# Kernel optimization log

Hardware: AMD Instinct MI355X
Metric: run time of the kernel (lower is better)

Reference implementation:

```python
import jax, jax.numpy as jnp
import numpy as np

B, T, D, H = 8, 2048, 512, 128

def setup_inputs() -> dict:
    key = jax.random.key(0)
    ks = jax.random.split(key, 8)
    s = lambda fan_in: 1.0 / np.sqrt(fan_in)
    return {
        "x": jax.random.normal(ks[0], (B, T, D), jnp.float32),
        "prediction": jax.random.normal(ks[1], (B, T, D), jnp.float32),
        "Wq": jax.random.uniform(ks[2], (D, H), jnp.float32, -s(D), s(D)),
        "bq": jnp.zeros((H,), jnp.float32),
        "Wk": jax.random.uniform(ks[3], (D, H), jnp.float32, -s(D), s(D)),
        "bk": jnp.zeros((H,), jnp.float32),
        "Wv": jax.random.uniform(ks[4], (D, D), jnp.float32, -s(D), s(D)),
        "bv": jnp.zeros((D,), jnp.float32),
        "Wf": jax.random.uniform(ks[5], (2 * D, D), jnp.float32, -s(2 * D), s(2 * D)),
        "bf": jnp.zeros((D,), jnp.float32),
    }

def reference(x, prediction, Wq, bq, Wk, bk, Wv, bv, Wf, bf):
    # q,k: [B,T,H]; v: [B,T,D]
    q = jnp.einsum('btd,dh->bth', prediction, Wq) + bq
    k = jnp.einsum('btd,dh->bth', x, Wk) + bk
    v = jnp.einsum('btd,de->bte', x, Wv) + bv
    # unscaled attention scores [B,T,T]
    scores = jnp.einsum('bth,bsh->bts', q, k)
    attn = jax.nn.softmax(scores, axis=-1)
    attended = jnp.einsum('bts,bsd->btd', attn, v)
    fusion_input = jnp.concatenate([prediction, attended], axis=-1)  # [B,T,2D]
    return jax.nn.sigmoid(jnp.einsum('btf,fd->btd', fusion_input, Wf) + bf)
```

## Files before the change

### kernel.cpp

```cpp
#include <hip/hip_runtime.h>
#include <hip/hip_bf16.h>


#define APF_B 8
#define APF_T 2048
#define APF_D 512
#define APF_H 128
#define APF_M (APF_B * APF_T)

typedef unsigned short u16;
typedef __attribute__((ext_vector_type(8))) short short8;
typedef __attribute__((ext_vector_type(4))) float f32x4;
typedef __attribute__((ext_vector_type(16))) float f32x16;

static __device__ __forceinline__ u16 f2bf(float x) {
    union { float f; unsigned int u; } cv;
    cv.f = x;
    unsigned int u = cv.u + 0x7FFFu + ((cv.u >> 16) & 1u);
    return (u16)(u >> 16);
}
static __device__ __forceinline__ u16 f2bf_hw(float x) {
    union { __hip_bfloat16 h; u16 u; } cv;
    cv.h = __float2bfloat16(x);
    return cv.u;
}

static __device__ __forceinline__ void load16_lds(const u16* g, u16* l) {
    __builtin_amdgcn_global_load_lds(
        (const __attribute__((address_space(1))) unsigned int*)g,
        (__attribute__((address_space(3))) unsigned int*)l,
        16, 0, 0);
}

static __device__ __forceinline__ f32x16 zero16() {
    f32x16 v;
#pragma unroll
    for (int i = 0; i < 16; ++i) v[i] = 0.f;
    return v;
}

__global__ __launch_bounds__(256) void prep_w(
    const float* __restrict__ Wq, u16* __restrict__ WqT,
    const float* __restrict__ Wk, u16* __restrict__ WkT,
    const float* __restrict__ Wv, u16* __restrict__ WvT,
    const float* __restrict__ Wf, u16* __restrict__ WfT)
{
    __shared__ float tile[64][65];
    int b = blockIdx.x;
    const float* src; u16* dst; int K, N;
    if (b < 16)      { src = Wq; dst = WqT; K = 512;  N = 128; }
    else if (b < 32) { b -= 16; src = Wk; dst = WkT; K = 512;  N = 128; }
    else if (b < 96) { b -= 32; src = Wv; dst = WvT; K = 512;  N = 512; }
    else             { b -= 96; src = Wf; dst = WfT; K = 1024; N = 512; }
    const int ntN = N >> 6;
    const int k0 = (b / ntN) * 64, n0 = (b % ntN) * 64;

    const int tid = threadIdx.x;
#pragma unroll
    for (int rep = 0; rep < 4; ++rep) {
        const int r = (tid >> 4) + rep * 16;
        const int c = (tid & 15) * 4;
        const float4 v = *(const float4*)&src[(long)(k0 + r) * N + n0 + c];
        tile[r][c] = v.x; tile[r][c + 1] = v.y;
        tile[r][c + 2] = v.z; tile[r][c + 3] = v.w;
    }
    __syncthreads();
#pragma unroll
    for (int rep = 0; rep < 2; ++rep) {
        const int rn = (tid >> 3) + rep * 32;
        const int ck = (tid & 7) * 8;
        short8 o;
#pragma unroll
        for (int j = 0; j < 8; ++j)
            o[j] = (short)f2bf_hw(tile[ck + j][rn]);
        *(short8*)&dst[(long)(n0 + rn) * K + k0 + ck] = o;
    }
}

template <int ADT, int BDT, int EPI, int BIASM, int VBLK>
static __device__ __forceinline__ void gemm_body(
    u16 (&smA)[2][4096], u16 (&smB)[2][4096],
    const void* Ap, long lda,
    const void* Bp, long ldb,
    const float* bias, void* Cp, long ldc, int K,
    long row0, long col0, const float* Cadd)
{
    const int tid  = threadIdx.x;
    const int lane = tid & 63;
    const int wid  = tid >> 6;
    const int wr   = wid >> 1;
    const int wc   = wid & 1;

    f32x4 acc[4][4];
#pragma unroll
    for (int i = 0; i < 4; ++i)
#pragma unroll
        for (int j = 0; j < 4; ++j)
            acc[i][j] = (f32x4){0.f, 0.f, 0.f, 0.f};

    const int lrow = (lane >> 4) * 4;
    const int lcol = lane & 15;
    const int q8   = (lane >> 4) * 8;

    float4 ra[2][2], rb[2][2];

    auto loadA = [&](int kb) {
        if (ADT == 1) {
            const float* Af = (const float*)Ap;
#pragma unroll
            for (int rep = 0; rep < 2; ++rep) {
                const int c = tid + rep * 256;
                const int rr = c >> 2, kc = (c & 3) * 8;
                const float* ga = Af + (row0 + rr) * lda + kb + kc;
                ra[rep][0] = *(const float4*)ga;
                ra[rep][1] = *(const float4*)(ga + 4);
            }
        }
    };
    auto loadB = [&](int kb) {
        if (BDT == 1) {
            const float* Bf = (const float*)Bp;
#pragma unroll
            for (int rep = 0; rep < 2; ++rep) {
                const int c = tid + rep * 256;
                const int rr = c >> 2, kc = (c & 3) * 8;
                const float* gb = Bf + (col0 + rr) * ldb + kb + kc;
                rb[rep][0] = *(const float4*)gb;
                rb[rep][1] = *(const float4*)(gb + 4);
            }
        }
    };
    auto dmaA = [&](int buf, int kb) {
        if (ADT == 0) {
            const u16* Ab = (const u16*)Ap;
#pragma unroll
            for (int rep = 0; rep < 2; ++rep) {
                const int c = tid + rep * 256;
                const int rr = c >> 2, kc = (c & 3) * 8;
                const int wbase = (wid * 64 + rep * 256) * 8;
                load16_lds(Ab + (row0 + rr) * lda + kb + kc, &smA[buf][wbase]);
            }
        }
    };
    auto dmaB = [&](int buf, int kb) {
        if (BDT == 0) {
            const u16* Bb = (const u16*)Bp;
#pragma unroll
            for (int rep = 0; rep < 2; ++rep) {
                const int c = tid + rep * 256;
                const int rr = c >> 2, kc = (c & 3) * 8;
                const int wbase = (wid * 64 + rep * 256) * 8;
                load16_lds(Bb + (col0 + rr) * ldb + kb + kc, &smB[buf][wbase]);
            }
        }
    };
    auto cvt8 = [&](const float4& a, const float4& b) {
        short8 v;
        v[0] = (short)f2bf_hw(a.x); v[1] = (short)f2bf_hw(a.y);
        v[2] = (short)f2bf_hw(a.z); v[3] = (short)f2bf_hw(a.w);
        v[4] = (short)f2bf_hw(b.x); v[5] = (short)f2bf_hw(b.y);
        v[6] = (short)f2bf_hw(b.z); v[7] = (short)f2bf_hw(b.w);
        return v;
    };
    auto writeA = [&](int buf) {
        if (ADT == 1) {
#pragma unroll
            for (int rep = 0; rep < 2; ++rep) {
                const int c = tid + rep * 256;
                *(short8*)&smA[buf][c * 8] = cvt8(ra[rep][0], ra[rep][1]);
            }
        }
    };
    auto writeB = [&](int buf) {
        if (BDT == 1) {
#pragma unroll
            for (int rep = 0; rep < 2; ++rep) {
                const int c = tid + rep * 256;
                *(short8*)&smB[buf][c * 8] = cvt8(rb[rep][0], rb[rep][1]);
            }
        }
    };

    const int NT = K / 32;
    loadA(0); loadB(0);
    writeA(0); writeB(0);
    dmaA(0, 0); dmaB(0, 0);

    int cur = 0;
    for (int t = 0; t < NT; ++t) {
        const int kb2 = (t + 1) * 32;
        if (t + 1 < NT) { loadA(kb2); loadB(kb2); }
        __syncthreads();
        if (t + 1 < NT) { dmaA(cur ^ 1, kb2); dmaB(cur ^ 1, kb2); }

        short8 av[4], bv4[4];
#pragma unroll
        for (int ti = 0; ti < 4; ++ti)
            av[ti] = *(const short8*)&smA[cur][(wr * 64 + ti * 16 + lcol) * 32 + q8];
#pragma unroll
        for (int tj = 0; tj < 4; ++tj)
            bv4[tj] = *(const short8*)&smB[cur][(wc * 64 + tj * 16 + lcol) * 32 + q8];

#pragma unroll
        for (int ti = 0; ti < 4; ++ti)
#pragma unroll
            for (int tj = 0; tj < 4; ++tj)
                acc[ti][tj] = __builtin_amdgcn_mfma_f32_16x16x32_bf16(
                    av[ti], bv4[tj], acc[ti][tj], 0, 0, 0);

        if (t + 1 < NT) { writeA(cur ^ 1); writeB(cur ^ 1); }
        cur ^= 1;
    }

#pragma unroll
    for (int ti = 0; ti < 4; ++ti) {
        const long m0t = row0 + wr * 64 + ti * 16 + lrow;
#pragma unroll
        for (int tj = 0; tj < 4; ++tj) {
            const long n = col0 + wc * 64 + tj * 16 + lcol;
            const float bn = (BIASM == 0 && bias != nullptr) ? bias[n] : 0.f;
            if (EPI == 0) {
                u16* C = (u16*)Cp;
#pragma unroll
                for (int r = 0; r < 4; ++r) {
                    const long m = m0t + r;
                    const float bm = (BIASM == 1) ? bias[m] : bn;
                    long idx;
                    if (VBLK) {
                        idx = ((((m >> 5) * 256) + (n >> 3)) << 8) +
                              ((m & 31) << 3) + (n & 7);
                    } else {
                        idx = m * ldc + n;
                    }
                    C[idx] = f2bf(acc[ti][tj][r] + bm);
                }
            } else if (EPI == 2) {
                float* C = (float*)Cp;
#pragma unroll
                for (int r = 0; r < 4; ++r) {
                    const float val = acc[ti][tj][r] + bn;
                    C[(m0t + r) * ldc + n] = 1.0f / (1.0f + expf(-val));
                }
            } else if (EPI == 3) {
                float* C = (float*)Cp;
#pragma unroll
                for (int r = 0; r < 4; ++r)
                    C[(m0t + r) * ldc + n] = acc[ti][tj][r] + bn;
            } else {
                float* C = (float*)Cp;
#pragma unroll
                for (int r = 0; r < 4; ++r) {
                    const float val = acc[ti][tj][r] + Cadd[(m0t + r) * ldc + n];
                    C[(m0t + r) * ldc + n] = 1.0f / (1.0f + expf(-val));
                }
            }
        }
    }
}

__global__ __launch_bounds__(256, 3) void mid_gemms(
    const float* __restrict__ x, const float* __restrict__ pred,
    const u16* __restrict__ WqT, const u16* __restrict__ WkT,
    const u16* __restrict__ WvT, const u16* __restrict__ WfT,
    const float* __restrict__ bq, const float* __restrict__ bk,
    const float* __restrict__ bv, const float* __restrict__ bfu,
    u16* __restrict__ qb, u16* __restrict__ kbuf, u16* __restrict__ vTb,
    float* __restrict__ Cpre)
{
    __shared__ u16 smA[2][4096];
    __shared__ u16 smB[2][4096];

    const int bid = blockIdx.x;
    if (bid < 256) {
        const int zz = bid >> 7, by = bid & 127;
        gemm_body<1, 0, 0, 0, 0>(smA, smB,
            zz ? (const void*)x : (const void*)pred, APF_D,
            zz ? WkT : WqT, APF_D,
            zz ? bk : bq, zz ? (void*)kbuf : (void*)qb, APF_H, APF_D,
            (long)by * 128, 0, nullptr);
    } else if (bid < 768) {
        const int t = bid - 256;
        const int zz = t >> 6, rem = t & 63;
        const int bx = rem & 15, by = rem >> 4;
        gemm_body<0, 1, 0, 1, 1>(smA, smB,
            WvT, APF_D,
            (const void*)(x + (long)zz * APF_T * APF_D), APF_D,
            bv, (void*)(vTb + (long)zz * 1048576L), APF_T, APF_D,
            (long)by * 128, (long)bx * 128, nullptr);
    } else {
        const int t = bid - 768;
        const int bx = t & 3, by = t >> 2;
        gemm_body<1, 0, 3, 0, 0>(smA, smB,
            (const void*)pred, APF_D,
            WfT, 1024,
            bfu, (void*)Cpre, APF_D, APF_D,
            (long)by * 128, (long)bx * 128, nullptr);
    }
}

__global__ __launch_bounds__(256, 2) void fusion_gemm(
    const u16* __restrict__ attb, const u16* __restrict__ WfT,
    const float* __restrict__ Cpre, float* __restrict__ out)
{
    __shared__ u16 smA[2][4096];
    __shared__ u16 smB[2][4096];
    gemm_body<0, 0, 4, 0, 0>(smA, smB,
        (const void*)attb, APF_D,
        WfT + 512, 1024,
        nullptr, (void*)out, APF_D, APF_D,
        (long)blockIdx.y * 128, (long)blockIdx.x * 128, Cpre);
}

__global__ __launch_bounds__(256, 3) void attn_fused(
    const u16* __restrict__ qg, const u16* __restrict__ kg,
    const u16* __restrict__ vTg, u16* __restrict__ attg)
{
    __shared__ u16 sQ[64 * 128];
    __shared__ u16 sK[64 * 128];
    __shared__ u16 sP[64 * 64];
    __shared__ float sRS[192];

    const int tid  = threadIdx.x;
    const int lane = tid & 63;
    const int w    = tid >> 6;
    const int l31  = lane & 31;
    const int hi   = lane >> 5;
    const int qb   = w >> 1;
    const int sb   = w & 1;

    const int  bid = blockIdx.x;
    const long z   = bid & 7;
    const int  r   = bid >> 3;
    const long q0  = (long)(r & 31) * 64;
    const long d0  = (long)(r >> 5) * 256;

    const u16* kbase0 = kg + z * (long)APF_T * APF_H;

    {
        const u16* qsrc = qg + (z * APF_T + q0) * APF_H;
#pragma unroll
        for (int rep = 0; rep < 4; ++rep) {
            const int c    = tid + rep * 256;
            const int row  = c >> 4;
            const int col8 = (c & 15) * 8;
            load16_lds(qsrc + row * APF_H + (col8 ^ ((row & 15) << 3)), &sQ[c * 8]);
        }
#pragma unroll
        for (int rep = 0; rep < 4; ++rep) {
            const int c    = tid + rep * 256;
            const int row  = c >> 4;
            const int col8 = (c & 15) * 8;
            load16_lds(kbase0 + row * APF_H + (col8 ^ ((row & 15) << 3)), &sK[c * 8]);
        }
    }
    __syncthreads();

    f32x16 oacc[2][2];
#pragma unroll
    for (int i = 0; i < 2; ++i)
#pragma unroll
        for (int j = 0; j < 2; ++j) oacc[i][j] = zero16();
    f32x16 rsacc = zero16();

    const long dblk0 = (d0 >> 5) + w * 2;
    const u16* vzb = vTg + z * 1048576L + dblk0 * 65536L + (long)l31 * 8;

    const int qrow = qb * 32 + l31;
    const int krow = sb * 32 + l31;
    const int pcol = sb * 32 + l31;

    for (int kt = 0; kt < APF_T / 64; ++kt) {
        f32x16 sacc = zero16();
#pragma unroll
        for (int ks = 0; ks < 8; ++ks) {
            const int colk = ks * 16 + hi * 8;
            const short8 av = *(const short8*)&sQ[qrow * 128 + (colk ^ ((qrow & 15) << 3))];
            const short8 bv = *(const short8*)&sK[krow * 128 + (colk ^ ((krow & 15) << 3))];
            sacc = __builtin_amdgcn_mfma_f32_32x32x16_bf16(av, bv, sacc, 0, 0, 0);
        }
        __syncthreads();

        if (kt + 1 < APF_T / 64) {
            const u16* ksrc = kbase0 + (long)(kt + 1) * 64 * APF_H;
#pragma unroll
            for (int rep = 0; rep < 4; ++rep) {
                const int c    = tid + rep * 256;
                const int row  = c >> 4;
                const int col8 = (c & 15) * 8;
                load16_lds(ksrc + row * APF_H + (col8 ^ ((row & 15) << 3)), &sK[c * 8]);
            }
        }

        const long sbase = (long)kt * 8 + hi;
        short8 vf1[2][2];
#pragma unroll
        for (int dt = 0; dt < 2; ++dt)
#pragma unroll
            for (int ks = 0; ks < 2; ++ks)
                vf1[dt][ks] = *(const short8*)(vzb + dt * 65536L + (sbase + ks * 2) * 256);

#pragma unroll
        for (int rg = 0; rg < 16; ++rg) {
            const float e = __expf(sacc[rg]);
            rsacc[rg] += e;
            const int prow = qb * 32 + (rg & 3) + 8 * (rg >> 2) + 4 * hi;
            sP[prow * 64 + (pcol ^ ((prow & 7) << 3))] = f2bf(e);
        }
        __syncthreads();

#pragma unroll
        for (int ks = 0; ks < 2; ++ks) {
            const int colk = ks * 16 + hi * 8;
            short8 pa[2];
#pragma unroll
            for (int qt = 0; qt < 2; ++qt) {
                const int prow = qt * 32 + l31;
                pa[qt] = *(const short8*)&sP[prow * 64 + (colk ^ ((prow & 7) << 3))];
            }
#pragma unroll
            for (int dt = 0; dt < 2; ++dt)
#pragma unroll
                for (int qt = 0; qt < 2; ++qt)
                    oacc[qt][dt] = __builtin_amdgcn_mfma_f32_32x32x16_bf16(
                        pa[qt], vf1[dt][ks], oacc[qt][dt], 0, 0, 0);
        }

        short8 vf2[2][2];
#pragma unroll
        for (int dt = 0; dt < 2; ++dt)
#pragma unroll
            for (int ks = 0; ks < 2; ++ks)
                vf2[dt][ks] = *(const short8*)(vzb + dt * 65536L + (sbase + (ks + 2) * 2) * 256);

#pragma unroll
        for (int ks = 0; ks < 2; ++ks) {
            const int colk = (ks + 2) * 16 + hi * 8;
            short8 pa[2];
#pragma unroll
            for (int qt = 0; qt < 2; ++qt) {
                const int prow = qt * 32 + l31;
                pa[qt] = *(const short8*)&sP[prow * 64 + (colk ^ ((prow & 7) << 3))];
            }
#pragma unroll
            for (int dt = 0; dt < 2; ++dt)
#pragma unroll
                for (int qt = 0; qt < 2; ++qt)
                    oacc[qt][dt] = __builtin_amdgcn_mfma_f32_32x32x16_bf16(
                        pa[qt], vf2[dt][ks], oacc[qt][dt], 0, 0, 0);
        }
    }

#pragma unroll
    for (int rg = 0; rg < 16; ++rg) {
        float s = rsacc[rg];
        s += __shfl_xor(s, 1);
        s += __shfl_xor(s, 2);
        s += __shfl_xor(s, 4);
        s += __shfl_xor(s, 8);
        s += __shfl_xor(s, 16);
        rsacc[rg] = s;
    }
    if (l31 == 0) {
#pragma unroll
        for (int rg = 0; rg < 16; ++rg) {
            const int row = (rg & 3) + 8 * (rg >> 2) + 4 * hi;
            sRS[w * 32 + row] = rsacc[rg];
        }
    }
    __syncthreads();
    if (tid < 64) {
        const int qb2 = tid >> 5, r2 = tid & 31;
        sRS[128 + tid] = 1.0f / (sRS[(qb2 * 2 + 0) * 32 + r2] +
                                 sRS[(qb2 * 2 + 1) * 32 + r2]);
    }
    __syncthreads();

    const long rowg0 = z * APF_T + q0;
    const long colg0 = d0 + (long)w * 64;
#pragma unroll
    for (int qt = 0; qt < 2; ++qt)
#pragma unroll
        for (int rg = 0; rg < 16; ++rg) {
            const int row = qt * 32 + (rg & 3) + 8 * (rg >> 2) + 4 * hi;
            const float inv = sRS[128 + row];
#pragma unroll
            for (int dt = 0; dt < 2; ++dt)
                attg[(rowg0 + row) * APF_D + colg0 + dt * 32 + l31] =
                    f2bf(oacc[qt][dt][rg] * inv);
        }
}

extern "C" void kernel_launch(void* const* d_in, const int* in_sizes, int n_in,
                              void* d_out, int out_size, void* d_ws, size_t ws_size,
                              hipStream_t stream)
{
    (void)in_sizes; (void)n_in; (void)out_size; (void)ws_size;

    const float* x    = (const float*)d_in[0];
    const float* pred = (const float*)d_in[1];
    const float* Wq   = (const float*)d_in[2];
    const float* bq   = (const float*)d_in[3];
    const float* Wk   = (const float*)d_in[4];
    const float* bk   = (const float*)d_in[5];
    const float* Wv   = (const float*)d_in[6];
    const float* bv   = (const float*)d_in[7];
    const float* Wf   = (const float*)d_in[8];
    const float* bfu  = (const float*)d_in[9];

    float* Cpre = (float*)d_ws;
    u16* wsp  = (u16*)(Cpre + (long)APF_M * APF_D);
    u16* qb   = wsp;
    u16* kbuf = qb   + (long)APF_M * APF_H;
    u16* vTb  = kbuf + (long)APF_M * APF_H;
    u16* attb = vTb  + (long)APF_M * APF_D;
    u16* WqT  = attb + (long)APF_M * APF_D;
    u16* WkT  = WqT  + (long)APF_H * APF_D;
    u16* WvT  = WkT  + (long)APF_H * APF_D;
    u16* WfT  = WvT  + (long)APF_D * APF_D;

    const dim3 thr(256);

    prep_w<<<dim3(224), thr, 0, stream>>>(Wq, WqT, Wk, WkT, Wv, WvT, Wf, WfT);

    mid_gemms<<<dim3(1280), thr, 0, stream>>>(
        x, pred, WqT, WkT, WvT, WfT, bq, bk, bv, bfu, qb, kbuf, vTb, Cpre);

    attn_fused<<<dim3(512), thr, 0, stream>>>(qb, kbuf, vTb, attb);

    fusion_gemm<<<dim3(4, 128), thr, 0, stream>>>(attb, WfT, Cpre,
                                                  (float*)d_out);
}
```

Measured before the change: 254.3 us.

## Double-buffer K and P tiles in attention, hold Q in registers, swizzle GEMM LDS

The attention kernel now keeps its Q fragments in registers instead of shared memory and double-buffers the K and P shared-memory tiles. This removes one of the two block barriers per key tile, and all V fragments are loaded in one batch. The GEMM body applies an XOR swizzle to its LDS tile layout for both DMA and converted stores, to cut bank conflicts on fragment reads. In exchange the attention kernel uses more registers and shared memory, and its launch bound drops from 3 to 2 blocks per CU.

```diff
diff --git a/kernel.cpp b/kernel.cpp
--- a/kernel.cpp
+++ b/kernel.cpp
@@ -7,6 +7,8 @@
 #define APF_D 512
 #define APF_H 128
 #define APF_M (APF_B * APF_T)
+
+#define GSWZ(row) ((((row) >> 1) & 3) << 3)
 
 typedef unsigned short u16;
 typedef __attribute__((ext_vector_type(8))) short short8;
@@ -138,7 +140,8 @@
                 const int c = tid + rep * 256;
                 const int rr = c >> 2, kc = (c & 3) * 8;
                 const int wbase = (wid * 64 + rep * 256) * 8;
-                load16_lds(Ab + (row0 + rr) * lda + kb + kc, &smA[buf][wbase]);
+                load16_lds(Ab + (row0 + rr) * lda + kb + (kc ^ GSWZ(rr)),
+                           &smA[buf][wbase]);
             }
         }
     };
@@ -150,7 +153,8 @@
                 const int c = tid + rep * 256;
                 const int rr = c >> 2, kc = (c & 3) * 8;
                 const int wbase = (wid * 64 + rep * 256) * 8;
-                load16_lds(Bb + (col0 + rr) * ldb + kb + kc, &smB[buf][wbase]);
+                load16_lds(Bb + (col0 + rr) * ldb + kb + (kc ^ GSWZ(rr)),
+                           &smB[buf][wbase]);
             }
         }
     };
@@ -167,7 +171,8 @@
 #pragma unroll
             for (int rep = 0; rep < 2; ++rep) {
                 const int c = tid + rep * 256;
-                *(short8*)&smA[buf][c * 8] = cvt8(ra[rep][0], ra[rep][1]);
+                *(short8*)&smA[buf][(c * 8) ^ GSWZ(c >> 2)] =
+                    cvt8(ra[rep][0], ra[rep][1]);
             }
         }
     };
@@ -176,7 +181,8 @@
 #pragma unroll
             for (int rep = 0; rep < 2; ++rep) {
                 const int c = tid + rep * 256;
-                *(short8*)&smB[buf][c * 8] = cvt8(rb[rep][0], rb[rep][1]);
+                *(short8*)&smB[buf][(c * 8) ^ GSWZ(c >> 2)] =
+                    cvt8(rb[rep][0], rb[rep][1]);
             }
         }
     };
@@ -195,11 +201,15 @@
 
         short8 av[4], bv4[4];
 #pragma unroll
-        for (int ti = 0; ti < 4; ++ti)
-            av[ti] = *(const short8*)&smA[cur][(wr * 64 + ti * 16 + lcol) * 32 + q8];
-#pragma unroll
-        for (int tj = 0; tj < 4; ++tj)
-            bv4[tj] = *(const short8*)&smB[cur][(wc * 64 + tj * 16 + lcol) * 32 + q8];
+        for (int ti = 0; ti < 4; ++ti) {
+            const int arow = wr * 64 + ti * 16 + lcol;
+            av[ti] = *(const short8*)&smA[cur][arow * 32 + (q8 ^ GSWZ(arow))];
+        }
+#pragma unroll
+        for (int tj = 0; tj < 4; ++tj) {
+            const int brow = wc * 64 + tj * 16 + lcol;
+            bv4[tj] = *(const short8*)&smB[cur][brow * 32 + (q8 ^ GSWZ(brow))];
+        }
 
 #pragma unroll
         for (int ti = 0; ti < 4; ++ti)
@@ -311,13 +321,12 @@
         (long)blockIdx.y * 128, (long)blockIdx.x * 128, Cpre);
 }
 
-__global__ __launch_bounds__(256, 3) void attn_fused(
+__global__ __launch_bounds__(256, 2) void attn_fused(
     const u16* __restrict__ qg, const u16* __restrict__ kg,
     const u16* __restrict__ vTg, u16* __restrict__ attg)
 {
-    __shared__ u16 sQ[64 * 128];
-    __shared__ u16 sK[64 * 128];
-    __shared__ u16 sP[64 * 64];
+    __shared__ u16 sK[2][64 * 128];
+    __shared__ u16 sP[2][64 * 64];
     __shared__ float sRS[192];
 
     const int tid  = threadIdx.x;
@@ -336,22 +345,21 @@
 
     const u16* kbase0 = kg + z * (long)APF_T * APF_H;
 
+#pragma unroll
+    for (int rep = 0; rep < 4; ++rep) {
+        const int c    = tid + rep * 256;
+        const int row  = c >> 4;
+        const int col8 = (c & 15) * 8;
+        load16_lds(kbase0 + row * APF_H + (col8 ^ ((row & 15) << 3)),
+                   &sK[0][c * 8]);
+    }
+
+    short8 qf[8];
     {
-        const u16* qsrc = qg + (z * APF_T + q0) * APF_H;
-#pragma unroll
-        for (int rep = 0; rep < 4; ++rep) {
-            const int c    = tid + rep * 256;
-            const int row  = c >> 4;
-            const int col8 = (c & 15) * 8;
-            load16_lds(qsrc + row * APF_H + (col8 ^ ((row & 15) << 3)), &sQ[c * 8]);
-        }
-#pragma unroll
-        for (int rep = 0; rep < 4; ++rep) {
-            const int c    = tid + rep * 256;
-            const int row  = c >> 4;
-            const int col8 = (c & 15) * 8;
-            load16_lds(kbase0 + row * APF_H + (col8 ^ ((row & 15) << 3)), &sK[c * 8]);
-        }
+        const u16* qsrc = qg + (z * APF_T + q0 + qb * 32 + l31) * APF_H;
+#pragma unroll
+        for (int ks = 0; ks < 8; ++ks)
+            qf[ks] = *(const short8*)(qsrc + ks * 16 + hi * 8);
     }
     __syncthreads();
 
@@ -365,20 +373,19 @@
     const long dblk0 = (d0 >> 5) + w * 2;
     const u16* vzb = vTg + z * 1048576L + dblk0 * 65536L + (long)l31 * 8;
 
-    const int qrow = qb * 32 + l31;
     const int krow = sb * 32 + l31;
     const int pcol = sb * 32 + l31;
 
+    int cur = 0;
     for (int kt = 0; kt < APF_T / 64; ++kt) {
         f32x16 sacc = zero16();
 #pragma unroll
         for (int ks = 0; ks < 8; ++ks) {
             const int colk = ks * 16 + hi * 8;
-            const short8 av = *(const short8*)&sQ[qrow * 128 + (colk ^ ((qrow & 15) << 3))];
-            const short8 bv = *(const short8*)&sK[krow * 128 + (colk ^ ((krow & 15) << 3))];
-            sacc = __builtin_amdgcn_mfma_f32_32x32x16_bf16(av, bv, sacc, 0, 0, 0);
-        }
-        __syncthreads();
+            const short8 bv =
+                *(const short8*)&sK[cur][krow * 128 + (colk ^ ((krow & 15) << 3))];
+            sacc = __builtin_amdgcn_mfma_f32_32x32x16_bf16(qf[ks], bv, sacc, 0, 0, 0);
+        }
 
         if (kt + 1 < APF_T / 64) {
             const u16* ksrc = kbase0 + (long)(kt + 1) * 64 * APF_H;
@@ -387,67 +394,45 @@
                 const int c    = tid + rep * 256;
                 const int row  = c >> 4;
                 const int col8 = (c & 15) * 8;
-                load16_lds(ksrc + row * APF_H + (col8 ^ ((row & 15) << 3)), &sK[c * 8]);
+                load16_lds(ksrc + row * APF_H + (col8 ^ ((row & 15) << 3)),
+                           &sK[cur ^ 1][c * 8]);
             }
         }
 
         const long sbase = (long)kt * 8 + hi;
-        short8 vf1[2][2];
+        short8 vf[2][4];
 #pragma unroll
         for (int dt = 0; dt < 2; ++dt)
 #pragma unroll
-            for (int ks = 0; ks < 2; ++ks)
-                vf1[dt][ks] = *(const short8*)(vzb + dt * 65536L + (sbase + ks * 2) * 256);
+            for (int ks = 0; ks < 4; ++ks)
+                vf[dt][ks] = *(const short8*)(vzb + dt * 65536L + (sbase + ks * 2) * 256);
 
 #pragma unroll
         for (int rg = 0; rg < 16; ++rg) {
             const float e = __expf(sacc[rg]);
             rsacc[rg] += e;
             const int prow = qb * 32 + (rg & 3) + 8 * (rg >> 2) + 4 * hi;
-            sP[prow * 64 + (pcol ^ ((prow & 7) << 3))] = f2bf(e);
+            sP[cur][prow * 64 + (pcol ^ ((prow & 7) << 3))] = f2bf(e);
         }
         __syncthreads();
 
 #pragma unroll
-        for (int ks = 0; ks < 2; ++ks) {
+        for (int ks = 0; ks < 4; ++ks) {
             const int colk = ks * 16 + hi * 8;
             short8 pa[2];
 #pragma unroll
             for (int qt = 0; qt < 2; ++qt) {
                 const int prow = qt * 32 + l31;
-                pa[qt] = *(const short8*)&sP[prow * 64 + (colk ^ ((prow & 7) << 3))];
+                pa[qt] = *(const short8*)&sP[cur][prow * 64 + (colk ^ ((prow & 7) << 3))];
             }
 #pragma unroll
             for (int dt = 0; dt < 2; ++dt)
 #pragma unroll
                 for (int qt = 0; qt < 2; ++qt)
                     oacc[qt][dt] = __builtin_amdgcn_mfma_f32_32x32x16_bf16(
-                        pa[qt], vf1[dt][ks], oacc[qt][dt], 0, 0, 0);
-        }
-
-        short8 vf2[2][2];
-#pragma unroll
-        for (int dt = 0; dt < 2; ++dt)
-#pragma unroll
-            for (int ks = 0; ks < 2; ++ks)
-                vf2[dt][ks] = *(const short8*)(vzb + dt * 65536L + (sbase + (ks + 2) * 2) * 256);
-
-#pragma unroll
-        for (int ks = 0; ks < 2; ++ks) {
-            const int colk = (ks + 2) * 16 + hi * 8;
-            short8 pa[2];
-#pragma unroll
-            for (int qt = 0; qt < 2; ++qt) {
-                const int prow = qt * 32 + l31;
-                pa[qt] = *(const short8*)&sP[prow * 64 + (colk ^ ((prow & 7) << 3))];
-            }
-#pragma unroll
-            for (int dt = 0; dt < 2; ++dt)
-#pragma unroll
-                for (int qt = 0; qt < 2; ++qt)
-                    oacc[qt][dt] = __builtin_amdgcn_mfma_f32_32x32x16_bf16(
-                        pa[qt], vf2[dt][ks], oacc[qt][dt], 0, 0, 0);
-        }
+                        pa[qt], vf[dt][ks], oacc[qt][dt], 0, 0, 0);
+        }
+        cur ^= 1;
     }
 
 #pragma unroll
```

Result: no change. 253.0 us (-0.5%).
